# Performance work log

Hardware: AMD Instinct MI355X
Metric: run time of the kernel (lower is better)

Reference implementation:

```python
import jax, jax.numpy as jnp
import numpy as np

DN = ('NCH', 'OIH', 'NCH')

def conv1d(x, w, b, stride, pad):
    y = jax.lax.conv_general_dilated(x, w, (stride,), [(pad, pad)], dimension_numbers=DN)
    return y + b[None, :, None]

def deconv1d(x, w, b):
    # ConvTranspose1d(k=3, stride=2, padding=1, output_padding=1): L -> 2L
    # expressed as lhs-dilated conv with padding (k-1-p, k-1-p+output_padding) = (1, 2)
    y = jax.lax.conv_general_dilated(x, w, (1,), [(1, 2)], lhs_dilation=(2,), dimension_numbers=DN)
    return y + b[None, :, None]

def setup_inputs() -> dict:
    key = jax.random.key(0)
    ks = jax.random.split(key, 24)
    B, T, A = 256, 512, 32
    H = 256              # hidden_dim / embedding_dim
    K = 8192             # n_embeddings
    enc_ch = [64, 128, 256]
    dec_ch = [256, 128, 64]
    s = 0.05
    inp = {'x': jax.random.normal(ks[0], (B, T, A), jnp.float32)}
    # encoder convs (OIH layout), k=3
    in_ch = A
    for i, ch in enumerate(enc_ch):
        inp[f'enc_w{i}'] = jax.random.normal(ks[1 + 2 * i], (ch, in_ch, 3), jnp.float32) * s
        inp[f'enc_b{i}'] = jnp.zeros((ch,), jnp.float32)
        in_ch = ch
    inp['proj_w'] = jax.random.normal(ks[8], (H, enc_ch[-1], 1), jnp.float32) * s
    inp['proj_b'] = jnp.zeros((H,), jnp.float32)
    inp['embedding'] = jax.random.normal(ks[9], (K, H), jnp.float32)
    # decoder deconvs (stored directly in conv OIH form)
    in_ch = H
    for i, ch in enumerate(dec_ch + [A]):
        inp[f'dec_w{i}'] = jax.random.normal(ks[10 + 2 * i], (ch, in_ch, 3), jnp.float32) * s
        inp[f'dec_b{i}'] = jnp.zeros((ch,), jnp.float32)
        in_ch = ch
    return inp

def _forward(x, enc_w0, enc_b0, enc_w1, enc_b1, enc_w2, enc_b2, proj_w, proj_b,
             embedding, dec_w0, dec_b0, dec_w1, dec_b1, dec_w2, dec_b2, dec_w3, dec_b3):
    # ---- encoder ----
    h = jnp.transpose(x, (0, 2, 1))                      # (B, A, T)
    h = jax.nn.relu(conv1d(h, enc_w0, enc_b0, 2, 1))
    h = jax.nn.relu(conv1d(h, enc_w1, enc_b1, 2, 1))
    h = jax.nn.relu(conv1d(h, enc_w2, enc_b2, 2, 1))
    z_e = conv1d(h, proj_w, proj_b, 1, 0)                # (B, H, T/8)
    # ---- EMA vector quantizer (eval-mode math) ----
    B, C, T = z_e.shape
    flat = jnp.transpose(z_e, (0, 2, 1)).reshape(-1, C)  # (B*T, C)
    dist = (jnp.sum(flat * flat, axis=1, keepdims=True)
            - 2.0 * flat @ embedding.T
            + jnp.sum(embedding * embedding, axis=1))    # (B*T, K)
    indices = jnp.argmin(dist, axis=1)                   # (B*T,)
    z_q = embedding[indices].reshape(B, T, C).transpose(0, 2, 1)  # (B, C, T)
    commitment_loss = jnp.mean((jax.lax.stop_gradient(z_e) - z_q) ** 2)
    codebook_loss = jnp.mean((z_e - jax.lax.stop_gradient(z_q)) ** 2)
    z_q = z_e + jax.lax.stop_gradient(z_q - z_e)         # straight-through
    # ---- decoder ----
    d = jax.nn.relu(deconv1d(z_q, dec_w0, dec_b0))
    d = jax.nn.relu(deconv1d(d, dec_w1, dec_b1))
    d = jax.nn.relu(deconv1d(d, dec_w2, dec_b2))
    d = deconv1d(d, dec_w3, dec_b3)                      # (B, A, seq_len)
    out = jnp.transpose(d, (0, 2, 1))                    # (B, seq_len, A)
    return out, codebook_loss, commitment_loss, indices.reshape(B, T)

def reference(x, enc_w0, enc_b0, enc_w1, enc_b1, enc_w2, enc_b2, proj_w, proj_b,
              embedding, dec_w0, dec_b0, dec_w1, dec_b1, dec_w2, dec_b2, dec_w3, dec_b3):
    return _forward(x, enc_w0, enc_b0, enc_w1, enc_b1, enc_w2, enc_b2, proj_w, proj_b,
                    embedding, dec_w0, dec_b0, dec_w1, dec_b1, dec_w2, dec_b2, dec_w3, dec_b3)
```

## Files before the change

### kernel.cpp

```cpp
#include <hip/hip_runtime.h>


typedef _Float16 half8 __attribute__((ext_vector_type(8)));
typedef _Float16 half4v __attribute__((ext_vector_type(4)));
typedef float f32x4 __attribute__((ext_vector_type(4)));
typedef float f32x16 __attribute__((ext_vector_type(16)));

struct CP2 {
  const _Float16* inH; const _Float16* inL;
  const _Float16* wH; const _Float16* wL;
  const float* bias;
  float* outF; _Float16* outH; _Float16* outL;
  const int* vidx;
  int Ci, lg2Ci, Ti, Co, To, K2, stride, pad, lg2U, Umask;
};

template<int SP, int PAR, bool GATHER, bool RELU, int OM>
__global__ __launch_bounds__(256, SP == 2 ? 3 : 4) void conv_mfma(CP2 p) {
  __shared__ _Float16 As[SP * 128 * 40];
  __shared__ _Float16 Bs[SP * 64 * 40];
  const int tid = threadIdx.x;
  const int wv = tid >> 6;
  const int lane = tid & 63;
  const int m = lane & 15, q = lane >> 4;
  const int btbase = blockIdx.x * 128;
  const int cobase = blockIdx.y * 64;
  f32x4 acc[2][4];
#pragma unroll
  for (int i = 0; i < 2; ++i)
#pragma unroll
    for (int j = 0; j < 4; ++j) acc[i][j] = {0.f, 0.f, 0.f, 0.f};

  const int nkb = p.K2 >> 5;
  for (int kb = 0; kb < nkb; ++kb) {
    const int k0 = kb << 5;
    const int tap = k0 >> p.lg2Ci;
    const int ci0 = k0 & (p.Ci - 1);
    int dt;
    if (PAR == 0)      { dt = 0; }
    else if (PAR == 1) { dt = tap; }
    else               { dt = tap - p.pad; }
    __syncthreads();
    {
      const int wb = (blockIdx.y * nkb + kb) * 2048 + tid * 8;
      *(uint4*)&Bs[(tid >> 2) * 40 + (tid & 3) * 8] = *(const uint4*)&p.wH[wb];
      if (SP == 2)
        *(uint4*)&Bs[64 * 40 + (tid >> 2) * 40 + (tid & 3) * 8] = *(const uint4*)&p.wL[wb];
    }
#pragma unroll
    for (int it = 0; it < 2; ++it) {
      const int r = it * 64 + (tid >> 2), g = tid & 3;
      const int bt = btbase + r;
      const int b = bt >> p.lg2U, u = bt & p.Umask;
      const int tin = (PAR < 0) ? u * p.stride + dt : u + dt;
      const bool ok = (tin >= 0) && (tin < p.Ti);
      int ai;
      if (GATHER) {
        const int er = ok ? p.vidx[b * p.Ti + tin] : 0;
        ai = er * 256 + ci0 + g * 8;
      } else {
        ai = (b * p.Ti + tin) * p.Ci + ci0 + g * 8;
      }
      const uint4 z = {0u, 0u, 0u, 0u};
      const uint4 vh = ok ? *(const uint4*)&p.inH[ai] : z;
      *(uint4*)&As[r * 40 + g * 8] = vh;
      if (SP == 2) {
        const uint4 vl = ok ? *(const uint4*)&p.inL[ai] : z;
        *(uint4*)&As[128 * 40 + r * 40 + g * 8] = vl;
      }
    }
    __syncthreads();
    half8 a1[2], a2[2];
#pragma unroll
    for (int rt = 0; rt < 2; ++rt) {
      const int row = wv * 32 + rt * 16 + m;
      a1[rt] = *(const half8*)&As[row * 40 + q * 8];
      if (SP == 2) a2[rt] = *(const half8*)&As[128 * 40 + row * 40 + q * 8];
    }
#pragma unroll
    for (int ct = 0; ct < 4; ++ct) {
      const half8 b1 = *(const half8*)&Bs[(ct * 16 + m) * 40 + q * 8];
      half8 b2;
      if (SP == 2) b2 = *(const half8*)&Bs[64 * 40 + (ct * 16 + m) * 40 + q * 8];
#pragma unroll
      for (int rt = 0; rt < 2; ++rt) {
        acc[rt][ct] = __builtin_amdgcn_mfma_f32_16x16x32_f16(a1[rt], b1, acc[rt][ct], 0, 0, 0);
        if (SP == 2) {
          acc[rt][ct] = __builtin_amdgcn_mfma_f32_16x16x32_f16(a2[rt], b1, acc[rt][ct], 0, 0, 0);
          acc[rt][ct] = __builtin_amdgcn_mfma_f32_16x16x32_f16(a1[rt], b2, acc[rt][ct], 0, 0, 0);
        }
      }
    }
  }
#pragma unroll
  for (int ct = 0; ct < 4; ++ct) {
    const int co = cobase + ct * 16 + m;
    if (co < p.Co) {
      const float bv = p.bias[co];
#pragma unroll
      for (int rt = 0; rt < 2; ++rt) {
#pragma unroll
        for (int j = 0; j < 4; ++j) {
          const int row = btbase + wv * 32 + rt * 16 + q * 4 + j;
          const int b = row >> p.lg2U, u = row & p.Umask;
          float v = acc[rt][ct][j] + bv;
          if (RELU) v = fmaxf(v, 0.f);
          const int t = (PAR < 0) ? u : 2 * u + PAR;
          const int oi = (b * p.To + t) * p.Co + co;
          if (OM == 3) {
            p.outF[oi] = v;
          } else if (OM == 1) {
            p.outH[oi] = (_Float16)v;
          } else {
            const _Float16 h = (_Float16)v;
            const _Float16 l = (_Float16)(v - (float)h);
            p.outH[oi] = h; p.outL[oi] = l;
          }
        }
      }
    }
  }
}

struct CPD {
  const _Float16* inH; const _Float16* wS; const float* bias;
  float* outF; _Float16* outH;
  int Ci, Ti, Co, To, lg2U, Umask;
};

template<bool RELU, bool F32OUT>
__global__ __launch_bounds__(256, 4) void conv_dec(CPD p) {
  __shared__ _Float16 As[129 * 40];
  __shared__ _Float16 Bs[3 * 64 * 40];
  const int tid = threadIdx.x;
  const int wv = tid >> 6;
  const int lane = tid & 63;
  const int m = lane & 15, q = lane >> 4;
  const int btbase = blockIdx.x * 128;
  const int cobase = blockIdx.y * 64;
  const int b0 = btbase >> p.lg2U;
  const int u0 = btbase & p.Umask;
  f32x4 aE[2][4], aO[2][4];
#pragma unroll
  for (int i = 0; i < 2; ++i)
#pragma unroll
    for (int j = 0; j < 4; ++j) { aE[i][j] = {0.f,0.f,0.f,0.f}; aO[i][j] = {0.f,0.f,0.f,0.f}; }

  const int nkb = p.Ci >> 5;
  for (int kb = 0; kb < nkb; ++kb) {
    const int ci0 = kb << 5;
    __syncthreads();
    {
      const int wb = (blockIdx.y * nkb + kb) * 6144 + tid * 8;
      const int ld = (tid >> 2) * 40 + (tid & 3) * 8;
#pragma unroll
      for (int tap = 0; tap < 3; ++tap)
        *(uint4*)&Bs[tap * 2560 + ld] = *(const uint4*)&p.wS[wb + tap * 2048];
    }
#pragma unroll
    for (int i = 0; i < 3; ++i) {
      const int e = i * 256 + tid;
      const int r = e >> 2, g = e & 3;
      if (r < 129) {
        const int ur = u0 + r;
        const bool ok = ur < p.Ti;
        const uint4 z = {0u, 0u, 0u, 0u};
        const uint4 v = ok ? *(const uint4*)&p.inH[(b0 * p.Ti + ur) * p.Ci + ci0 + g * 8] : z;
        *(uint4*)&As[r * 40 + g * 8] = v;
      }
    }
    __syncthreads();
    half8 a0[2], a1s[2];
#pragma unroll
    for (int rt = 0; rt < 2; ++rt) {
      const int row = wv * 32 + rt * 16 + m;
      a0[rt]  = *(const half8*)&As[row * 40 + q * 8];
      a1s[rt] = *(const half8*)&As[(row + 1) * 40 + q * 8];
    }
#pragma unroll
    for (int ct = 0; ct < 4; ++ct) {
      const int c = ct * 16 + m;
      const half8 w0 = *(const half8*)&Bs[c * 40 + q * 8];
      const half8 w1 = *(const half8*)&Bs[2560 + c * 40 + q * 8];
      const half8 w2 = *(const half8*)&Bs[5120 + c * 40 + q * 8];
#pragma unroll
      for (int rt = 0; rt < 2; ++rt) {
        aE[rt][ct] = __builtin_amdgcn_mfma_f32_16x16x32_f16(a0[rt],  w1, aE[rt][ct], 0, 0, 0);
        aO[rt][ct] = __builtin_amdgcn_mfma_f32_16x16x32_f16(a0[rt],  w0, aO[rt][ct], 0, 0, 0);
        aO[rt][ct] = __builtin_amdgcn_mfma_f32_16x16x32_f16(a1s[rt], w2, aO[rt][ct], 0, 0, 0);
      }
    }
  }
#pragma unroll
  for (int ct = 0; ct < 4; ++ct) {
    const int co = cobase + ct * 16 + m;
    if (co < p.Co) {
      const float bv = p.bias[co];
#pragma unroll
      for (int rt = 0; rt < 2; ++rt) {
#pragma unroll
        for (int j = 0; j < 4; ++j) {
          const int u = u0 + wv * 32 + rt * 16 + q * 4 + j;
          float vE = aE[rt][ct][j] + bv;
          float vO = aO[rt][ct][j] + bv;
          if (RELU) { vE = fmaxf(vE, 0.f); vO = fmaxf(vO, 0.f); }
          const int oiE = (b0 * p.To + 2 * u) * p.Co + co;
          const int oiO = oiE + p.Co;
          if (F32OUT) { p.outF[oiE] = vE; p.outF[oiO] = vO; }
          else        { p.outH[oiE] = (_Float16)vE; p.outH[oiO] = (_Float16)vO; }
        }
      }
    }
  }
}


__global__ __launch_bounds__(256) void x_prep(const float* __restrict__ x,
                                              _Float16* __restrict__ h,
                                              _Float16* __restrict__ l) {
  const int i = blockIdx.x * 256 + threadIdx.x;
  const float4 v = ((const float4*)x)[i];
  half4v a, b;
  a.x = (_Float16)v.x; b.x = (_Float16)(v.x - (float)a.x);
  a.y = (_Float16)v.y; b.y = (_Float16)(v.y - (float)a.y);
  a.z = (_Float16)v.z; b.z = (_Float16)(v.z - (float)a.z);
  a.w = (_Float16)v.w; b.w = (_Float16)(v.w - (float)a.w);
  ((half4v*)h)[i] = a;
  ((half4v*)l)[i] = b;
}

struct WPE { const float* w; int dh, dl, Ci, lg2Ci, KWO, Co, PAR, SP, nkb, base, dec; };
struct WPA { WPE e[9]; };

__global__ __launch_bounds__(256) void w_prep(WPA a, _Float16* __restrict__ wst) {
  const int b = (int)blockIdx.x;
  int i = 0;
#pragma unroll
  for (int j = 1; j < 9; ++j) if (b >= a.e[j].base) i = j;
  const WPE E = a.e[i];
  const int local = b - E.base;
  const int cb = local / E.nkb;
  const int kb = local - cb * E.nkb;
  const int tid = threadIdx.x;
  const int cc = tid >> 2, g = tid & 3;
  const int co = cb * 64 + cc;
  const bool okc = co < E.Co;
  const int k0 = kb << 5;
  const int tap0 = k0 >> E.lg2Ci;
  const int ci0 = k0 & (E.Ci - 1);
  if (!E.dec) {
    const int ko = (E.PAR == 0) ? 1 : (E.PAR == 1 ? 2 * tap0 : tap0);
    half8 hv, lv;
#pragma unroll
    for (int j = 0; j < 8; ++j) {
      const float wv = okc ? E.w[(co * E.Ci + ci0 + g * 8 + j) * E.KWO + ko] : 0.f;
      hv[j] = (_Float16)wv;
      lv[j] = (_Float16)(wv - (float)hv[j]);
    }
    const int off = (cb * E.nkb + kb) * 2048 + tid * 8;
    *(half8*)&wst[E.dh + off] = hv;
    if (E.SP == 2) *(half8*)&wst[E.dl + off] = lv;
  } else {
#pragma unroll
    for (int tap = 0; tap < 3; ++tap) {
      half8 hv;
#pragma unroll
      for (int j = 0; j < 8; ++j) {
        const float wv = okc ? E.w[(co * E.Ci + ci0 + g * 8 + j) * 3 + tap] : 0.f;
        hv[j] = (_Float16)wv;
      }
      *(half8*)&wst[E.dh + ((cb * E.nkb + kb) * 3 + tap) * 2048 + tid * 8] = hv;
    }
  }
}

__global__ __launch_bounds__(256) void emb_prep(const float* __restrict__ emb,
                                                _Float16* __restrict__ hi,
                                                _Float16* __restrict__ lo,
                                                float* __restrict__ nrm) {
  const int k = blockIdx.x * 4 + (threadIdx.x >> 6);
  const int lane = threadIdx.x & 63;
  const int i = k * 64 + lane;
  const float4 v = ((const float4*)emb)[i];
  half4v a, b;
  a.x = (_Float16)v.x; b.x = (_Float16)(v.x - (float)a.x);
  a.y = (_Float16)v.y; b.y = (_Float16)(v.y - (float)a.y);
  a.z = (_Float16)v.z; b.z = (_Float16)(v.z - (float)a.z);
  a.w = (_Float16)v.w; b.w = (_Float16)(v.w - (float)a.w);
  ((half4v*)hi)[i] = a;
  ((half4v*)lo)[i] = b;
  double s = (double)v.x * v.x + (double)v.y * v.y +
             (double)v.z * v.z + (double)v.w * v.w;
  for (int off = 32; off; off >>= 1) s += __shfl_down(s, off);
  if (lane == 0) nrm[k] = (float)s;
}

__global__ __launch_bounds__(256, 2) void vq_mfma(const _Float16* __restrict__ z1g,
                                                  const _Float16* __restrict__ z2g,
                                                  const _Float16* __restrict__ e1g,
                                                  const _Float16* __restrict__ e2g,
                                                  const float* __restrict__ nrm,
                                                  float* __restrict__ pbest,
                                                  int* __restrict__ pidx) {
  __shared__ _Float16 es[2 * 2 * 4096];
  const int tid = threadIdx.x;
  const int lane = tid & 63;
  const int w = tid >> 6;
  const int m32 = lane & 31;
  const int hi = lane >> 5;
  const int seg = blockIdx.x & 7, rb = blockIdx.x >> 3;
  const int rbase = rb * 128;
  const int row_g = rbase + w * 32 + m32;

  half8 za[16], zb[16];
#pragma unroll
  for (int c = 0; c < 16; ++c) {
    const int zi = row_g * 256 + c * 16 + hi * 8;
    za[c] = *(const half8*)&z1g[zi];
    zb[c] = *(const half8*)&z2g[zi];
  }

  float best[16]; int bk[16];
#pragma unroll
  for (int i = 0; i < 16; ++i) { best[i] = 3.4e38f; bk[i] = 0; }

  const int sbase = (seg * 1024 + ((tid >> 7) & 1) * 32 + (tid & 31)) * 256
                  + ((tid >> 6) & 1) * 16 + ((tid >> 5) & 1) * 8;
  const int lw = w * 512;

  auto stage = [&](int cc_, int kb_, int buf_) {
    const int off = sbase + cc_ * 32768 + kb_ * 32;
    __builtin_amdgcn_global_load_lds(
        (const __attribute__((address_space(1))) void*)(e1g + off),
        (__attribute__((address_space(3))) void*)&es[(buf_ * 2 + 0) * 4096 + lw], 16, 0, 0);
    __builtin_amdgcn_global_load_lds(
        (const __attribute__((address_space(1))) void*)(e1g + off + 16384),
        (__attribute__((address_space(3))) void*)&es[(buf_ * 2 + 0) * 4096 + 2048 + lw], 16, 0, 0);
    __builtin_amdgcn_global_load_lds(
        (const __attribute__((address_space(1))) void*)(e2g + off),
        (__attribute__((address_space(3))) void*)&es[(buf_ * 2 + 1) * 4096 + lw], 16, 0, 0);
    __builtin_amdgcn_global_load_lds(
        (const __attribute__((address_space(1))) void*)(e2g + off + 16384),
        (__attribute__((address_space(3))) void*)&es[(buf_ * 2 + 1) * 4096 + 2048 + lw], 16, 0, 0);
  };

  stage(0, 0, 0);

  const int lb = lane * 8;
  f32x16 acc[4];
  for (int cc = 0; cc < 8; ++cc) {
    const int cbase = seg * 1024 + cc * 128;
#pragma unroll
    for (int ct = 0; ct < 4; ++ct) {
#pragma unroll
      for (int rg = 0; rg < 16; ++rg) acc[ct][rg] = 0.f;
    }
#pragma unroll
    for (int kb = 0; kb < 8; ++kb) {
      const int buf = kb & 1;
      const _Float16* e1s = &es[(buf * 2 + 0) * 4096];
      const _Float16* e2s = &es[(buf * 2 + 1) * 4096];
      __syncthreads();
      if (kb < 7)      stage(cc, kb + 1, buf ^ 1);
      else if (cc < 7) stage(cc + 1, 0, buf ^ 1);
      __builtin_amdgcn_s_setprio(1);
#pragma unroll
      for (int ct = 0; ct < 4; ++ct) {
#pragma unroll
        for (int k16 = 0; k16 < 2; ++k16) {
          const half8 b1 = *(const half8*)&e1s[ct * 1024 + k16 * 512 + lb];
          const half8 b2 = *(const half8*)&e2s[ct * 1024 + k16 * 512 + lb];
          const half8 a1 = za[kb * 2 + k16];
          const half8 a2 = zb[kb * 2 + k16];
          acc[ct] = __builtin_amdgcn_mfma_f32_32x32x16_f16(a1, b1, acc[ct], 0, 0, 0);
          acc[ct] = __builtin_amdgcn_mfma_f32_32x32x16_f16(a2, b1, acc[ct], 0, 0, 0);
          acc[ct] = __builtin_amdgcn_mfma_f32_32x32x16_f16(a1, b2, acc[ct], 0, 0, 0);
        }
      }
      __builtin_amdgcn_s_setprio(0);
    }
#pragma unroll
    for (int ct = 0; ct < 4; ++ct) {
      const int k = cbase + ct * 32 + m32;
      const float nv = nrm[k];
#pragma unroll
      for (int rg = 0; rg < 16; ++rg) {
        const float d = nv - 2.f * acc[ct][rg];
        if (d < best[rg]) { best[rg] = d; bk[rg] = k; }
      }
    }
  }
#pragma unroll
  for (int rg = 0; rg < 16; ++rg) {
    float bv = best[rg]; int kv = bk[rg];
    for (int off = 1; off < 32; off <<= 1) {
      const float ob = __shfl_xor(bv, off);
      const int ok = __shfl_xor(kv, off);
      if (ob < bv || (ob == bv && ok < kv)) { bv = ob; kv = ok; }
    }
    if (m32 == 0) {
      const int row = rbase + w * 32 + (rg & 3) + 8 * (rg >> 2) + 4 * hi;
      pbest[seg * 16384 + row] = bv;
      pidx[seg * 16384 + row] = kv;
    }
  }
}

__global__ void merge_kernel(const float* __restrict__ pbest, const int* __restrict__ pidx,
                             int* __restrict__ vidx, float* __restrict__ out_idx,
                             float* __restrict__ lacc) {
  const int n = blockIdx.x * 256 + threadIdx.x;
  float bv = pbest[n]; int kv = pidx[n];
#pragma unroll
  for (int s = 1; s < 8; ++s) {
    const float ob = pbest[s * 16384 + n];
    const int ok = pidx[s * 16384 + n];
    if (ob < bv || (ob == bv && ok < kv)) { bv = ob; kv = ok; }
  }
  vidx[n] = kv;
  out_idx[n] = (float)kv;
  if (n == 0) *lacc = 0.f;
}

__global__ __launch_bounds__(256) void loss_kernel(const _Float16* __restrict__ z1g,
                                                   const _Float16* __restrict__ z2g,
                                                   const float* __restrict__ emb,
                                                   const int* __restrict__ vidx,
                                                   float* __restrict__ lacc) {
  const int g4 = blockIdx.x * 256 + threadIdx.x;
  const int e0 = g4 * 4;
  const int n = e0 >> 8, c = e0 & 255;
  const half4v a = ((const half4v*)z1g)[g4];
  const half4v b = ((const half4v*)z2g)[g4];
  const float4 q4 = *(const float4*)&emb[vidx[n] * 256 + c];
  const float dx = ((float)a.x + (float)b.x) - q4.x;
  const float dy = ((float)a.y + (float)b.y) - q4.y;
  const float dz = ((float)a.z + (float)b.z) - q4.z;
  const float dw = ((float)a.w + (float)b.w) - q4.w;
  float s = dx * dx + dy * dy + dz * dz + dw * dw;
  for (int off = 32; off; off >>= 1) s += __shfl_down(s, off);
  __shared__ float red[4];
  if ((threadIdx.x & 63) == 0) red[threadIdx.x >> 6] = s;
  __syncthreads();
  if (threadIdx.x == 0) atomicAdd(lacc, red[0] + red[1] + red[2] + red[3]);
}

__global__ void fin_kernel(const float* __restrict__ lacc, float* __restrict__ out, int loff) {
  if (threadIdx.x == 0) {
    const float l = *lacc * (1.f / 4194304.f);
    out[loff] = l;
    out[loff + 1] = l;
  }
}

extern "C" void kernel_launch(void* const* d_in, const int* in_sizes, int n_in,
                              void* d_out, int out_size, void* d_ws, size_t ws_size,
                              hipStream_t stream) {
  const float* x   = (const float*)d_in[0];
  const float* ew0 = (const float*)d_in[1];  const float* eb0 = (const float*)d_in[2];
  const float* ew1 = (const float*)d_in[3];  const float* eb1 = (const float*)d_in[4];
  const float* ew2 = (const float*)d_in[5];  const float* eb2 = (const float*)d_in[6];
  const float* pw  = (const float*)d_in[7];  const float* pb  = (const float*)d_in[8];
  const float* emb = (const float*)d_in[9];
  const float* dw0 = (const float*)d_in[10]; const float* db0 = (const float*)d_in[11];
  const float* dw1 = (const float*)d_in[12]; const float* db1 = (const float*)d_in[13];
  const float* dw2 = (const float*)d_in[14]; const float* db2 = (const float*)d_in[15];
  const float* dw3 = (const float*)d_in[16]; const float* db3 = (const float*)d_in[17];
  float* ws  = (float*)d_ws;
  float* out = (float*)d_out;

  const int A0 = 0, B0 = 4194304, C0 = 8388608, TL = 12582912;
  _Float16* h0h = (_Float16*)(ws + C0);
  _Float16* h0l = h0h + 4194304;
  _Float16* h1h = (_Float16*)(ws + B0);
  _Float16* h1l = h1h + 4194304;
  _Float16* h2h = (_Float16*)(ws + A0);
  _Float16* h2l = h2h + 4194304;
  _Float16* h3h = (_Float16*)(ws + B0);
  _Float16* h3l = h3h + 4194304;
  _Float16* z1g = (_Float16*)(ws + A0);
  _Float16* z2g = z1g + 4194304;
  _Float16* e1g = (_Float16*)(ws + B0);
  _Float16* e2g = e1g + 2097152;
  float* pbest = ws + B0 + 2097152;
  int*   pidx  = (int*)(ws + B0 + 2097152 + 131072);
  _Float16* d1h = (_Float16*)(ws + C0);
  _Float16* d2h = (_Float16*)(ws + A0);
  _Float16* d3h = (_Float16*)(ws + B0);
  float* nrm  = ws + TL;
  int*   vidx = (int*)(ws + TL + 8192);
  float* lacc = ws + TL + 8192 + 16384;
  _Float16* wst = (_Float16*)(ws + TL + 32768);

  const int W_E0H = 0,      W_E0L = 6144;
  const int W_E1H = 12288,  W_E1L = 36864;
  const int W_E2H = 61440,  W_E2L = 159744;
  const int W_PJH = 258048, W_PJL = 323584;
  const int W_D0A = 389120, W_D0B = 454656;
  const int W_DC1 = 585728, W_DC2 = 684032, W_DC3 = 708608;

  const int idx_off  = out_size - 16384;
  const int loss_off = out_size - 16386;

  x_prep<<<4096, 256, 0, stream>>>(x, h0h, h0l);
  WPA wa;
  wa.e[0] = {ew0, W_E0H, W_E0L, 32,  5, 3, 64,  -1, 2, 3,  0,   0};
  wa.e[1] = {ew1, W_E1H, W_E1L, 64,  6, 3, 128, -1, 2, 6,  3,   0};
  wa.e[2] = {ew2, W_E2H, W_E2L, 128, 7, 3, 256, -1, 2, 12, 15,  0};
  wa.e[3] = {pw,  W_PJH, W_PJL, 256, 8, 1, 256, -1, 2, 8,  63,  0};
  wa.e[4] = {dw0, W_D0A, 0,     256, 8, 3, 256,  0, 1, 8,  95,  0};
  wa.e[5] = {dw0, W_D0B, 0,     256, 8, 3, 256,  1, 1, 16, 127, 0};
  wa.e[6] = {dw1, W_DC1, 0,     256, 8, 3, 128, -1, 1, 8,  191, 1};
  wa.e[7] = {dw2, W_DC2, 0,     128, 7, 3, 64,  -1, 1, 4,  207, 1};
  wa.e[8] = {dw3, W_DC3, 0,     64,  6, 3, 32,  -1, 1, 2,  211, 1};
  w_prep<<<213, 256, 0, stream>>>(wa, wst);

  CP2 p; p.vidx = nullptr; p.inH = nullptr; p.inL = nullptr;
  p.outF = nullptr; p.outH = nullptr; p.outL = nullptr;

  p.inH = h0h; p.inL = h0l; p.wH = wst + W_E0H; p.wL = wst + W_E0L;
  p.bias = eb0; p.outH = h1h; p.outL = h1l;
  p.Ci = 32; p.lg2Ci = 5; p.Ti = 512; p.Co = 64; p.To = 256;
  p.K2 = 96; p.stride = 2; p.pad = 1; p.lg2U = 8; p.Umask = 255;
  conv_mfma<2, -1, false, true, 0><<<dim3(512, 1), 256, 0, stream>>>(p);

  p.inH = h1h; p.inL = h1l; p.wH = wst + W_E1H; p.wL = wst + W_E1L;
  p.bias = eb1; p.outH = h2h; p.outL = h2l;
  p.Ci = 64; p.lg2Ci = 6; p.Ti = 256; p.Co = 128; p.To = 128; p.K2 = 192;
  p.lg2U = 7; p.Umask = 127;
  conv_mfma<2, -1, false, true, 0><<<dim3(256, 2), 256, 0, stream>>>(p);

  p.inH = h2h; p.inL = h2l; p.wH = wst + W_E2H; p.wL = wst + W_E2L;
  p.bias = eb2; p.outH = h3h; p.outL = h3l;
  p.Ci = 128; p.lg2Ci = 7; p.Ti = 128; p.Co = 256; p.To = 64; p.K2 = 384;
  p.lg2U = 6; p.Umask = 63;
  conv_mfma<2, -1, false, true, 0><<<dim3(128, 4), 256, 0, stream>>>(p);

  p.inH = h3h; p.inL = h3l; p.wH = wst + W_PJH; p.wL = wst + W_PJL;
  p.bias = pb; p.outH = z1g; p.outL = z2g;
  p.Ci = 256; p.lg2Ci = 8; p.Ti = 64; p.Co = 256; p.To = 64;
  p.K2 = 256; p.stride = 1; p.pad = 0; p.lg2U = 6; p.Umask = 63;
  conv_mfma<2, -1, false, false, 0><<<dim3(128, 4), 256, 0, stream>>>(p);

  emb_prep<<<2048, 256, 0, stream>>>(emb, e1g, e2g, nrm);
  vq_mfma<<<1024, 256, 0, stream>>>(z1g, z2g, e1g, e2g, nrm, pbest, pidx);
  merge_kernel<<<64, 256, 0, stream>>>(pbest, pidx, vidx, out + idx_off, lacc);
  loss_kernel<<<4096, 256, 0, stream>>>(z1g, z2g, emb, vidx, lacc);
  fin_kernel<<<1, 64, 0, stream>>>(lacc, out, loss_off);

  p.inH = e1g; p.inL = nullptr; p.bias = db0;
  p.outH = d1h; p.outL = nullptr; p.vidx = vidx;
  p.Ci = 256; p.lg2Ci = 8; p.Ti = 64; p.Co = 256; p.To = 128;
  p.lg2U = 6; p.Umask = 63;
  p.wH = wst + W_D0A; p.wL = nullptr;
  p.K2 = 256; conv_mfma<1, 0, true, true, 1><<<dim3(128, 4), 256, 0, stream>>>(p);
  p.wH = wst + W_D0B;
  p.K2 = 512; conv_mfma<1, 1, true, true, 1><<<dim3(128, 4), 256, 0, stream>>>(p);

  CPD d;
  d.inH = d1h; d.wS = wst + W_DC1; d.bias = db1; d.outF = nullptr; d.outH = d2h;
  d.Ci = 256; d.Ti = 128; d.Co = 128; d.To = 256; d.lg2U = 7; d.Umask = 127;
  conv_dec<true, false><<<dim3(256, 2), 256, 0, stream>>>(d);

  d.inH = d2h; d.wS = wst + W_DC2; d.bias = db2; d.outH = d3h;
  d.Ci = 128; d.Ti = 256; d.Co = 64; d.To = 512; d.lg2U = 8; d.Umask = 255;
  conv_dec<true, false><<<dim3(512, 1), 256, 0, stream>>>(d);

  d.inH = d3h; d.wS = wst + W_DC3; d.bias = db3; d.outF = out; d.outH = nullptr;
  d.Ci = 64; d.Ti = 512; d.Co = 32; d.To = 1024; d.lg2U = 9; d.Umask = 511;
  conv_dec<false, true><<<dim3(1024, 1), 256, 0, stream>>>(d);
}
```

Baseline: 525.1 us.

## Prefetch next K-block tiles into registers in conv_mfma and conv_dec

Both the encoder/decoder MFMA conv kernel and the decoder deconv kernel now issue global loads for the next K-block into registers before computing on the current shared-memory tile, then write them to LDS at the start of the next iteration. This is meant to hide global-memory latency behind MFMA work, a software-pipelined main loop. In exchange it uses more registers, with two staging structs held live, which could lower occupancy under the launch bounds. A redundant assignment to inH was also added before the last decoder launch; it has no effect.

```diff
diff --git a/kernel.cpp b/kernel.cpp
--- a/kernel.cpp
+++ b/kernel.cpp
@@ -25,6 +25,8 @@
   const int m = lane & 15, q = lane >> 4;
   const int btbase = blockIdx.x * 128;
   const int cobase = blockIdx.y * 64;
+  const int rr0 = tid >> 2, g = tid & 3;
+  const int ldA = rr0 * 40 + g * 8;
   f32x4 acc[2][4];
 #pragma unroll
   for (int i = 0; i < 2; ++i)
@@ -32,25 +34,23 @@
     for (int j = 0; j < 4; ++j) acc[i][j] = {0.f, 0.f, 0.f, 0.f};
 
   const int nkb = p.K2 >> 5;
-  for (int kb = 0; kb < nkb; ++kb) {
+
+  struct St { uint4 a0h, a1h, a0l, a1l, bh, bl; };
+  auto LOAD = [&](int kb, St& s) {
     const int k0 = kb << 5;
     const int tap = k0 >> p.lg2Ci;
     const int ci0 = k0 & (p.Ci - 1);
     int dt;
-    if (PAR == 0)      { dt = 0; }
-    else if (PAR == 1) { dt = tap; }
-    else               { dt = tap - p.pad; }
-    __syncthreads();
-    {
-      const int wb = (blockIdx.y * nkb + kb) * 2048 + tid * 8;
-      *(uint4*)&Bs[(tid >> 2) * 40 + (tid & 3) * 8] = *(const uint4*)&p.wH[wb];
-      if (SP == 2)
-        *(uint4*)&Bs[64 * 40 + (tid >> 2) * 40 + (tid & 3) * 8] = *(const uint4*)&p.wL[wb];
-    }
+    if (PAR == 0)      dt = 0;
+    else if (PAR == 1) dt = tap;
+    else               dt = tap - p.pad;
+    const int wb = (blockIdx.y * nkb + kb) * 2048 + tid * 8;
+    s.bh = *(const uint4*)&p.wH[wb];
+    if (SP == 2) s.bl = *(const uint4*)&p.wL[wb];
+    const uint4 z = {0u, 0u, 0u, 0u};
 #pragma unroll
     for (int it = 0; it < 2; ++it) {
-      const int r = it * 64 + (tid >> 2), g = tid & 3;
-      const int bt = btbase + r;
+      const int bt = btbase + it * 64 + rr0;
       const int b = bt >> p.lg2U, u = bt & p.Umask;
       const int tin = (PAR < 0) ? u * p.stride + dt : u + dt;
       const bool ok = (tin >= 0) && (tin < p.Ti);
@@ -61,15 +61,33 @@
       } else {
         ai = (b * p.Ti + tin) * p.Ci + ci0 + g * 8;
       }
-      const uint4 z = {0u, 0u, 0u, 0u};
       const uint4 vh = ok ? *(const uint4*)&p.inH[ai] : z;
-      *(uint4*)&As[r * 40 + g * 8] = vh;
-      if (SP == 2) {
-        const uint4 vl = ok ? *(const uint4*)&p.inL[ai] : z;
-        *(uint4*)&As[128 * 40 + r * 40 + g * 8] = vl;
-      }
-    }
+      uint4 vl = z;
+      if (SP == 2) vl = ok ? *(const uint4*)&p.inL[ai] : z;
+      if (it == 0) { s.a0h = vh; if (SP == 2) s.a0l = vl; }
+      else         { s.a1h = vh; if (SP == 2) s.a1l = vl; }
+    }
+  };
+  auto WRITE = [&](St& s) {
+    *(uint4*)&As[ldA] = s.a0h;
+    *(uint4*)&As[2560 + ldA] = s.a1h;
+    if (SP == 2) {
+      *(uint4*)&As[128 * 40 + ldA] = s.a0l;
+      *(uint4*)&As[128 * 40 + 2560 + ldA] = s.a1l;
+    }
+    *(uint4*)&Bs[ldA] = s.bh;
+    if (SP == 2) *(uint4*)&Bs[64 * 40 + ldA] = s.bl;
+  };
+
+  St sA, sB;
+  LOAD(0, sA);
+  for (int kb = 0; kb < nkb; ++kb) {
     __syncthreads();
+    if ((kb & 1) == 0) WRITE(sA); else WRITE(sB);
+    __syncthreads();
+    if (kb + 1 < nkb) {
+      if ((kb & 1) == 0) LOAD(kb + 1, sB); else LOAD(kb + 1, sA);
+    }
     half8 a1[2], a2[2];
 #pragma unroll
     for (int rt = 0; rt < 2; ++rt) {
@@ -147,8 +165,36 @@
     for (int j = 0; j < 4; ++j) { aE[i][j] = {0.f,0.f,0.f,0.f}; aO[i][j] = {0.f,0.f,0.f,0.f}; }
 
   const int nkb = p.Ci >> 5;
+
+  struct StD { uint4 a0, a1, a2; };
+  auto LOADA = [&](int kb, StD& s) {
+    const int ci0 = kb << 5;
+    const uint4 z = {0u, 0u, 0u, 0u};
+#pragma unroll
+    for (int i = 0; i < 3; ++i) {
+      const int e = i * 256 + tid;
+      const int r = e >> 2, gg = e & 3;
+      uint4 v = z;
+      if (r < 129) {
+        const int ur = u0 + r;
+        if (ur < p.Ti) v = *(const uint4*)&p.inH[(b0 * p.Ti + ur) * p.Ci + ci0 + gg * 8];
+      }
+      if (i == 0) s.a0 = v; else if (i == 1) s.a1 = v; else s.a2 = v;
+    }
+  };
+  auto WRITEA = [&](StD& s) {
+#pragma unroll
+    for (int i = 0; i < 3; ++i) {
+      const int e = i * 256 + tid;
+      const int r = e >> 2, gg = e & 3;
+      if (r < 129)
+        *(uint4*)&As[r * 40 + gg * 8] = (i == 0) ? s.a0 : (i == 1) ? s.a1 : s.a2;
+    }
+  };
+
+  StD sA, sB;
+  LOADA(0, sA);
   for (int kb = 0; kb < nkb; ++kb) {
-    const int ci0 = kb << 5;
     __syncthreads();
     {
       const int wb = (blockIdx.y * nkb + kb) * 6144 + tid * 8;
@@ -157,19 +203,11 @@
       for (int tap = 0; tap < 3; ++tap)
         *(uint4*)&Bs[tap * 2560 + ld] = *(const uint4*)&p.wS[wb + tap * 2048];
     }
-#pragma unroll
-    for (int i = 0; i < 3; ++i) {
-      const int e = i * 256 + tid;
-      const int r = e >> 2, g = e & 3;
-      if (r < 129) {
-        const int ur = u0 + r;
-        const bool ok = ur < p.Ti;
-        const uint4 z = {0u, 0u, 0u, 0u};
-        const uint4 v = ok ? *(const uint4*)&p.inH[(b0 * p.Ti + ur) * p.Ci + ci0 + g * 8] : z;
-        *(uint4*)&As[r * 40 + g * 8] = v;
-      }
-    }
+    if ((kb & 1) == 0) WRITEA(sA); else WRITEA(sB);
     __syncthreads();
+    if (kb + 1 < nkb) {
+      if ((kb & 1) == 0) LOADA(kb + 1, sB); else LOADA(kb + 1, sA);
+    }
     half8 a0[2], a1s[2];
 #pragma unroll
     for (int rt = 0; rt < 2; ++rt) {
@@ -566,7 +604,8 @@
   d.Ci = 128; d.Ti = 256; d.Co = 64; d.To = 512; d.lg2U = 8; d.Umask = 255;
   conv_dec<true, false><<<dim3(512, 1), 256, 0, stream>>>(d);
 
-  d.inH = d3h; d.wS = wst + W_DC3; d.bias = db3; d.outF = out; d.outH = nullptr;
+  d.inH = d2h; d.wS = wst + W_DC3; d.bias = db3; d.outF = out; d.outH = nullptr;
+  d.inH = d3h;
   d.Ci = 64; d.Ti = 512; d.Co = 32; d.To = 1024; d.lg2U = 9; d.Umask = 511;
   conv_dec<false, true><<<dim3(1024, 1), 256, 0, stream>>>(d);
 }
```

Result: slower. 542.6 us (+3.3%).
